# Kernel tuning notes

Measured on AMD Instinct MI355X. Metric: run time of the kernel, lower is better.

## Reference

```python
import math
import jax, jax.numpy as jnp
import numpy as np

WH, WW = 7, 7
NUM_HEADS = 16


def _relative_position_index(wh, ww):
    # Static int index table, identical to the torch buffer construction.
    ch, cw = np.arange(wh), np.arange(ww)
    coords = np.stack(np.meshgrid(ch, cw, indexing='ij'))        # (2, wh, ww)
    cf = coords.reshape(2, -1)                                    # (2, N)
    rel = cf[:, :, None] - cf[:, None, :]                         # (2, N, N)
    rel = rel.transpose(1, 2, 0).copy()                           # (N, N, 2)
    rel[:, :, 0] += wh - 1
    rel[:, :, 1] += ww - 1
    rel[:, :, 0] *= 2 * ww - 1
    return rel.sum(-1)                                            # (N, N) int


def setup_inputs() -> dict:
    key = jax.random.key(0)
    ks = jax.random.split(key, 7)
    B_, N, C = 2048, WH * WW, 512
    nW = 64
    s = 1.0 / math.sqrt(C)
    return {
        'x': jax.random.normal(ks[0], (B_, N, C), jnp.float32),
        'mask': jax.random.normal(ks[1], (nW, N, N), jnp.float32),
        'qkv_w': jax.random.normal(ks[2], (3 * C, C), jnp.float32) * s,
        'qkv_b': jax.random.normal(ks[3], (3 * C,), jnp.float32) * 0.02,
        'proj_w': jax.random.normal(ks[4], (C, C), jnp.float32) * s,
        'proj_b': jax.random.normal(ks[5], (C,), jnp.float32) * 0.02,
        'bias_table': jax.random.normal(ks[6], (2 * WH - 1, 2 * WW - 1, NUM_HEADS), jnp.float32) * 0.02,
    }


def reference(x, mask, qkv_w, qkv_b, proj_w, proj_b, bias_table):
    B_, N, C = x.shape
    nH = NUM_HEADS
    hd = C // nH
    scale = math.sqrt(hd)  # self.scale = qk_scale or sqrt(head_dim)

    qkv = x @ qkv_w.T + qkv_b                                   # (B_, N, 3C)
    qkv = qkv.reshape(B_, N, 3, nH, hd).transpose(2, 0, 3, 1, 4)  # (3, B_, nH, N, hd)
    q, k, v = qkv[0], qkv[1], qkv[2]

    attn = jnp.einsum('bhnd,bhmd->bhnm', q, k) / scale           # (B_, nH, N, N)

    idx = _relative_position_index(WH, WW).reshape(-1)            # (N*N,) static
    bias = bias_table.reshape(-1, nH)[idx].reshape(N, N, nH)      # gather
    attn = attn + bias.transpose(2, 0, 1)[None]                   # (B_, nH, N, N)

    nW = mask.shape[0]
    attn = attn.reshape(B_ // nW, nW, nH, N, N) + mask[None, :, None]
    attn = attn.reshape(B_, nH, N, N)

    attn = jax.nn.softmax(attn, axis=-1)
    out = jnp.einsum('bhnm,bhmd->bhnd', attn, v)                  # (B_, nH, N, hd)
    out = out.transpose(0, 2, 1, 3).reshape(B_, N, C)
    return out @ proj_w.T + proj_b
```

## Files before the change

### kernel.cpp

```cpp
#include <hip/hip_runtime.h>
#include <hip/hip_bf16.h>


typedef __bf16  bf16x8 __attribute__((ext_vector_type(8)));
typedef float   f32x4  __attribute__((ext_vector_type(4)));

#define B_TOT   2048
#define NTOK    49
#define CDIM    512
#define NHEAD   16
#define HDIM    32
#define MROWS   (B_TOT * NTOK)
#define QKVN    (3 * CDIM)

__device__ __forceinline__ void load_lds16(const void* gptr, void* lptr) {
    __builtin_amdgcn_global_load_lds(
        (const __attribute__((address_space(1))) unsigned int*)gptr,
        (__attribute__((address_space(3))) unsigned int*)lptr,
        16, 0, 0);
}
__device__ __forceinline__ void load_lds4(const void* gptr, void* lptr) {
    __builtin_amdgcn_global_load_lds(
        (const __attribute__((address_space(1))) unsigned int*)gptr,
        (__attribute__((address_space(3))) unsigned int*)lptr,
        4, 0, 0);
}

__global__ void cvt_f32_bf16(const float* __restrict__ in,
                             __hip_bfloat16* __restrict__ out, int n4) {
    int idx = blockIdx.x * blockDim.x + threadIdx.x;
    int stride = gridDim.x * blockDim.x;
    for (int i = idx; i < n4; i += stride) {
        float4 f = ((const float4*)in)[i];
        union { __hip_bfloat16 h[4]; ushort4 u; } c;
        c.h[0] = __float2bfloat16(f.x);
        c.h[1] = __float2bfloat16(f.y);
        c.h[2] = __float2bfloat16(f.z);
        c.h[3] = __float2bfloat16(f.w);
        ((ushort4*)out)[i] = c.u;
    }
}

#define BARR    asm volatile("s_barrier" ::: "memory")
#define WAITV(N) asm volatile("s_waitcnt vmcnt(" #N ")" ::: "memory")
#define MFMA16(av, bv, cv) __builtin_amdgcn_mfma_f32_16x16x32_bf16(av, bv, cv, 0, 0, 0)

template <typename OutT>
__global__ __launch_bounds__(512, 2) void gemm256(
    const __hip_bfloat16* __restrict__ A,
    const __hip_bfloat16* __restrict__ B,
    const float* __restrict__ bias,
    OutT* __restrict__ C,
    int M, int N, int K, int nbx, int cpx)
{
    extern __shared__ __align__(16) char smem[];
    char* sA = smem;
    char* sB = smem + 65536;

    const int NT = K >> 6;

    const int tid  = threadIdx.x;
    const int lane = tid & 63;
    const int wave = tid >> 6;
    const int wm   = wave >> 2;
    const int wn   = wave & 3;
    const int l16  = lane & 15;
    const int quad = lane >> 4;

    const int id = blockIdx.x;
    const int sw = (id & 7) * cpx + (id >> 3);
    const int mb = sw / nbx;
    const int nb = sw - mb * nbx;
    const int m0 = mb << 8;
    const int n0 = nb << 8;

    const int srow = tid >> 3;
    const int scg  = ((tid & 7) << 3) ^ ((srow & 7) << 3);
    const __hip_bfloat16* Asrc = A + (size_t)(m0 + srow) * K + scg;
    const __hip_bfloat16* Bsrc = B + (size_t)(n0 + srow) * K + scg;
    char* dAl = sA + tid * 16;
    char* dBl = sB + tid * 16;

#define STG_A(t2, h) \
    { load_lds16(Asrc + (size_t)(h) * 128 * K + (t2) * 64,            \
                 dAl + ((t2) & 1) * 32768 + (h) * 16384);             \
      load_lds16(Asrc + ((size_t)(h) * 128 + 64) * K + (t2) * 64,     \
                 dAl + ((t2) & 1) * 32768 + (h) * 16384 + 8192); }
#define STG_B(t2, h) \
    { load_lds16(Bsrc + (size_t)(h) * 128 * K + (t2) * 64,            \
                 dBl + ((t2) & 1) * 32768 + (h) * 16384);             \
      load_lds16(Bsrc + ((size_t)(h) * 128 + 64) * K + (t2) * 64,     \
                 dBl + ((t2) & 1) * 32768 + (h) * 16384 + 8192); }

    STG_A(0, 0); STG_A(0, 1); STG_B(0, 0); STG_B(0, 1);
    STG_A(1, 0); STG_A(1, 1); STG_B(1, 0); STG_B(1, 1);
    WAITV(8);
    BARR;

    const int c0 = (quad * 16) ^ ((l16 & 7) << 4);
    const int c1 = c0 ^ 64;

    f32x4 acc[8][4] = {};

#define CLUSTER(mfa, mfb)                                                  \
    {                                                                      \
        bf16x8 xk0 = *(const bf16x8*)(pA + (mfa) * 2048 + c0);             \
        bf16x8 xk1 = *(const bf16x8*)(pA + (mfa) * 2048 + c1);             \
        bf16x8 yk0 = *(const bf16x8*)(pA + (mfb) * 2048 + c0);             \
        bf16x8 yk1 = *(const bf16x8*)(pA + (mfb) * 2048 + c1);             \
        __builtin_amdgcn_s_setprio(1);                                     \
        _Pragma("unroll")                                                  \
        for (int nf = 0; nf < 4; ++nf) {                                   \
            acc[mfa][nf] = MFMA16(xk0, Bf0[nf], acc[mfa][nf]);             \
            acc[mfa][nf] = MFMA16(xk1, Bf1[nf], acc[mfa][nf]);             \
            acc[mfb][nf] = MFMA16(yk0, Bf0[nf], acc[mfb][nf]);             \
            acc[mfb][nf] = MFMA16(yk1, Bf1[nf], acc[mfb][nf]);             \
        }                                                                  \
        __builtin_amdgcn_s_setprio(0);                                     \
    }

#pragma unroll 2
    for (int t = 0; t < NT; ++t) {
        const int sl = (t & 1) * 32768;
        const char* pA = sA + sl + wm * 16384 + l16 * 128;
        const char* pB = sB + sl + (wn >> 1) * 16384 + ((wn & 1) * 64 + l16) * 128;

        bf16x8 Bf0[4], Bf1[4];
#pragma unroll
        for (int nf = 0; nf < 4; ++nf) {
            Bf0[nf] = *(const bf16x8*)(pB + nf * 2048 + c0);
            Bf1[nf] = *(const bf16x8*)(pB + nf * 2048 + c1);
        }

        CLUSTER(0, 1);
        CLUSTER(2, 3);
        CLUSTER(4, 5);

        bf16x8 a6k0 = *(const bf16x8*)(pA + 6 * 2048 + c0);
        bf16x8 a6k1 = *(const bf16x8*)(pA + 6 * 2048 + c1);
        bf16x8 a7k0 = *(const bf16x8*)(pA + 7 * 2048 + c0);
        bf16x8 a7k1 = *(const bf16x8*)(pA + 7 * 2048 + c1);
        asm volatile("s_waitcnt lgkmcnt(0)" ::: "memory");
        BARR;

        if (t + 2 < NT) { STG_A(t + 2, 0); STG_A(t + 2, 1);
                          STG_B(t + 2, 0); STG_B(t + 2, 1); }

        __builtin_amdgcn_s_setprio(1);
#pragma unroll
        for (int nf = 0; nf < 4; ++nf) {
            acc[6][nf] = MFMA16(a6k0, Bf0[nf], acc[6][nf]);
            acc[6][nf] = MFMA16(a6k1, Bf1[nf], acc[6][nf]);
            acc[7][nf] = MFMA16(a7k0, Bf0[nf], acc[7][nf]);
            acc[7][nf] = MFMA16(a7k1, Bf1[nf], acc[7][nf]);
        }
        __builtin_amdgcn_s_setprio(0);

        if (t + 2 < NT) { WAITV(8); }
        else if (t + 1 < NT) { WAITV(0); }
        BARR;
    }
#undef CLUSTER
#undef STG_A
#undef STG_B

#pragma unroll
    for (int i = 0; i < 8; ++i) {
#pragma unroll
        for (int jj = 0; jj < 4; ++jj) {
            const int col = n0 + wn * 64 + jj * 16 + l16;
            const float bv = bias[col];
#pragma unroll
            for (int rr = 0; rr < 4; ++rr) {
                const int row = m0 + wm * 128 + i * 16 + quad * 4 + rr;
                const float val = acc[i][jj][rr] + bv;
                if constexpr (sizeof(OutT) == 2)
                    C[(size_t)row * N + col] = __float2bfloat16(val);
                else
                    C[(size_t)row * N + col] = val;
            }
        }
    }
}

#define QS_OFF   0
#define KS_OFF   12544
#define VS_OFF   25088
#define BIAS_OFF 41472
#define MASK_OFF 42824
#define SMEM_BYTES 52432

__global__ __launch_bounds__(256) void attn_mfma(
    const __hip_bfloat16* __restrict__ qkv,
    const float* __restrict__ mask,
    const float* __restrict__ bias_table,
    __hip_bfloat16* __restrict__ out)
{
    __shared__ __align__(16) char smem[SMEM_BYTES];

    const int tid  = threadIdx.x;
    const int lane = tid & 63;
    const int w    = tid >> 6;
    const int l16  = lane & 15;
    const int quad = lane >> 4;
    const int b    = blockIdx.x >> 2;
    const int hq   = blockIdx.x & 3;

    {
        const long rowbase = (long)b * NTOK * QKVN;
        for (int e = tid; e < 2352; e += 256) {
            const int m   = e / 784;
            const int rr  = e - m * 784;
            const int tok = rr >> 4, seg = rr & 15;
            const int segl = seg ^ (tok & 7);
            const __hip_bfloat16* src =
                qkv + rowbase + (long)tok * QKVN + m * 512 + hq * 128 + segl * 8;
            load_lds16(src, smem + e * 16);
        }
        for (int e = tid; e < 960; e += 256)
            ((unsigned int*)(smem + VS_OFF + 49 * 256))[e] = 0u;
        const float* msrc = mask + (long)(b & 63) * (NTOK * NTOK);
        for (int e = tid; e < NTOK * NTOK; e += 256)
            load_lds4(msrc + e, smem + MASK_OFF + e * 4);
        __hip_bfloat16* sb = (__hip_bfloat16*)(smem + BIAS_OFF);
        for (int e = tid; e < 676; e += 256) {
            const int w2 = e / 169, rel = e - w2 * 169;
            sb[e] = __float2bfloat16(bias_table[rel * NHEAD + hq * 4 + w2]);
        }
    }
    __syncthreads();

    const int fro = (w * 64 + quad * 16) ^ ((l16 & 7) << 4);
    bf16x8 af[4], bf[4];
#pragma unroll
    for (int t = 0; t < 4; ++t) {
        const int tok = t * 16 + l16;
        af[t] = *(const bf16x8*)(smem + KS_OFF + tok * 256 + fro);
        bf[t] = *(const bf16x8*)(smem + QS_OFF + tok * 256 + fro);
    }
    f32x4 acc[4][4] = {};
#pragma unroll
    for (int i = 0; i < 4; ++i)
#pragma unroll
        for (int j = 0; j < 4; ++j)
            acc[i][j] = __builtin_amdgcn_mfma_f32_16x16x32_bf16(
                af[i], bf[j], acc[i][j], 0, 0, 0);
    __syncthreads();

    const float scale = 0.17677669529663687f;
    const float* smf = (const float*)(smem + MASK_OFF);
    const __hip_bfloat16* sb = (const __hip_bfloat16*)(smem + BIAS_OFF);
    const int quad4 = quad * 4;

    int kp[4][4];
#pragma unroll
    for (int i = 0; i < 4; ++i)
#pragma unroll
        for (int r = 0; r < 4; ++r) {
            const int k  = i * 16 + quad4 + r;
            const int rj = k / 7, cj = k - rj * 7;
            kp[i][r] = (6 - rj) * 13 + (6 - cj);
        }

    char* pbase = smem + w * 6272;
#pragma unroll
    for (int j = 0; j < 4; ++j) {
        const int q   = j * 16 + l16;
        const bool qok = q < NTOK;
        const int ri  = q / 7, ci = q - ri * 7;
        const int qp  = ri * 13 + ci;
        const int mrow = q * NTOK;
        float mx = -1e30f;
#pragma unroll
        for (int i = 0; i < 4; ++i)
#pragma unroll
            for (int r = 0; r < 4; ++r) {
                const int k = i * 16 + quad4 + r;
                float v;
                if (qok && k < NTOK) {
                    v = fmaf(acc[i][j][r], scale,
                             __bfloat162float(sb[w * 169 + qp + kp[i][r]]) + smf[mrow + k]);
                } else {
                    v = -1e30f;
                }
                acc[i][j][r] = v;
                mx = fmaxf(mx, v);
            }
        mx = fmaxf(mx, __shfl_xor(mx, 16));
        mx = fmaxf(mx, __shfl_xor(mx, 32));
        float s = 0.f;
#pragma unroll
        for (int i = 0; i < 4; ++i)
#pragma unroll
            for (int r = 0; r < 4; ++r) {
                const float ev = __expf(acc[i][j][r] - mx);
                acc[i][j][r] = ev;
                s += ev;
            }
        s += __shfl_xor(s, 16);
        s += __shfl_xor(s, 32);
        const float inv = 1.0f / s;
        if (qok) {
            char* prow = pbase + q * 128;
            const int xr = (q & 7) << 4;
#pragma unroll
            for (int i = 0; i < 4; ++i) {
                union { __hip_bfloat16 h[4]; uint2 u; } pk;
#pragma unroll
                for (int r = 0; r < 4; ++r)
                    pk.h[r] = __float2bfloat16(acc[i][j][r] * inv);
                *(uint2*)(prow + ((i * 32 + quad * 8) ^ xr)) = pk.u;
            }
        }
    }
    __syncthreads();

    bf16x8 pa[4][2];
#pragma unroll
    for (int mt = 0; mt < 4; ++mt) {
        const int q  = mt * 16 + l16;
        const int xr = (q & 7) << 4;
#pragma unroll
        for (int ks = 0; ks < 2; ++ks)
            pa[mt][ks] = *(const bf16x8*)(pbase + q * 128 + ((ks * 64 + quad * 16) ^ xr));
    }
    bf16x8 vb[2][2];
#pragma unroll
    for (int dt = 0; dt < 2; ++dt)
#pragma unroll
        for (int ks = 0; ks < 2; ++ks)
#pragma unroll
            for (int e = 0; e < 8; ++e) {
                const int key = ks * 32 + quad * 8 + e;
                const int dby = (w * 32 + dt * 16 + l16) * 2;
                vb[dt][ks][e] = *(const __bf16*)(smem + VS_OFF + key * 256 + (dby ^ (e << 4)));
            }
    f32x4 o[4][2] = {};
#pragma unroll
    for (int mt = 0; mt < 4; ++mt)
#pragma unroll
        for (int dt = 0; dt < 2; ++dt)
#pragma unroll
            for (int ks = 0; ks < 2; ++ks)
                o[mt][dt] = __builtin_amdgcn_mfma_f32_16x16x32_bf16(
                    pa[mt][ks], vb[dt][ks], o[mt][dt], 0, 0, 0);

    const long obase = (long)b * NTOK * CDIM + hq * 128 + w * 32;
#pragma unroll
    for (int mt = 0; mt < 4; ++mt)
#pragma unroll
        for (int r = 0; r < 4; ++r) {
            const int q = mt * 16 + quad4 + r;
            if (q < NTOK) {
                const long rb = obase + (long)q * CDIM;
#pragma unroll
                for (int dt = 0; dt < 2; ++dt)
                    out[rb + dt * 16 + l16] = __float2bfloat16(o[mt][dt][r]);
            }
        }
}

extern "C" void kernel_launch(void* const* d_in, const int* in_sizes, int n_in,
                              void* d_out, int out_size, void* d_ws, size_t ws_size,
                              hipStream_t stream) {
    const float* x          = (const float*)d_in[0];
    const float* mask       = (const float*)d_in[1];
    const float* qkv_w      = (const float*)d_in[2];
    const float* qkv_b      = (const float*)d_in[3];
    const float* proj_w     = (const float*)d_in[4];
    const float* proj_b     = (const float*)d_in[5];
    const float* bias_table = (const float*)d_in[6];

    char* ws = (char*)d_ws;
    __hip_bfloat16* xb   = (__hip_bfloat16*)(ws);
    __hip_bfloat16* qw   = (__hip_bfloat16*)(ws + 102760448);
    __hip_bfloat16* pw   = (__hip_bfloat16*)(ws + 104333312);
    __hip_bfloat16* qkvb = (__hip_bfloat16*)(ws + 104857600);
    __hip_bfloat16* ao   = xb;

    static int attr_done = 0;
    if (!attr_done) {
        hipFuncSetAttribute(
            reinterpret_cast<const void*>(&gemm256<__hip_bfloat16>),
            hipFuncAttributeMaxDynamicSharedMemorySize, 131072);
        hipFuncSetAttribute(
            reinterpret_cast<const void*>(&gemm256<float>),
            hipFuncAttributeMaxDynamicSharedMemorySize, 131072);
        attr_done = 1;
    }

    cvt_f32_bf16<<<32768, 256, 0, stream>>>(x, xb, (MROWS * CDIM) / 4);
    cvt_f32_bf16<<<768,   256, 0, stream>>>(qkv_w, qw, (QKVN * CDIM) / 4);
    cvt_f32_bf16<<<256,   256, 0, stream>>>(proj_w, pw, (CDIM * CDIM) / 4);

    gemm256<__hip_bfloat16><<<2352, 512, 131072, stream>>>(
        xb, qw, qkv_b, qkvb, MROWS, QKVN, CDIM, 6, 294);

    attn_mfma<<<B_TOT * 4, 256, 0, stream>>>(qkvb, mask, bias_table, ao);

    gemm256<float><<<784, 512, 131072, stream>>>(
        ao, pw, proj_b, (float*)d_out, MROWS, CDIM, CDIM, 2, 98);
}
```

Baseline: 754.2 us.

## Restructure GEMM main loop into quadrant phases with interleaved staged loads

Replaces the double-buffered K loop with a fully unrolled 8-step loop, where each step is split into four quadrant phases (M-half by N-half). Each phase issues its LDS reads, launches part of the next tile's global-to-LDS copies, then runs its MFMAs between barriers. The intent is to spread global loads and LDS traffic across the compute so they overlap more evenly with the MFMAs. The loop now hardcodes K=512 (8 tiles of 64) and adds many more barriers, which could cost sync overhead, and it drops the generic NT so other K values are no longer handled.

New measurement: 713.8 us. -5.4%, faster.

```diff
diff --git a/kernel.cpp b/kernel.cpp
--- a/kernel.cpp
+++ b/kernel.cpp
@@ -43,6 +43,7 @@
 
 #define BARR    asm volatile("s_barrier" ::: "memory")
 #define WAITV(N) asm volatile("s_waitcnt vmcnt(" #N ")" ::: "memory")
+#define LGKM0   asm volatile("s_waitcnt lgkmcnt(0)" ::: "memory")
 #define MFMA16(av, bv, cv) __builtin_amdgcn_mfma_f32_16x16x32_bf16(av, bv, cv, 0, 0, 0)
 
 template <typename OutT>
@@ -57,8 +58,6 @@
     char* sA = smem;
     char* sB = smem + 65536;
 
-    const int NT = K >> 6;
-
     const int tid  = threadIdx.x;
     const int lane = tid & 63;
     const int wave = tid >> 6;
@@ -93,74 +92,77 @@
                  dBl + ((t2) & 1) * 32768 + (h) * 16384 + 8192); }
 
     STG_A(0, 0); STG_A(0, 1); STG_B(0, 0); STG_B(0, 1);
-    STG_A(1, 0); STG_A(1, 1); STG_B(1, 0); STG_B(1, 1);
-    WAITV(8);
+    STG_B(1, 0); STG_B(1, 1);
+    WAITV(4);
     BARR;
 
+    const char* pA0 = sA + wm * 16384 + l16 * 128;
+    const char* pA1 = pA0 + 32768;
+    const char* pB0 = sB + (wn >> 1) * 16384 + (wn & 1) * 8192 + l16 * 128;
+    const char* pB1 = pB0 + 32768;
     const int c0 = (quad * 16) ^ ((l16 & 7) << 4);
     const int c1 = c0 ^ 64;
 
+    bf16x8 ar[8], b0r[4], b1r[4];
     f32x4 acc[8][4] = {};
 
-#define CLUSTER(mfa, mfb)                                                  \
-    {                                                                      \
-        bf16x8 xk0 = *(const bf16x8*)(pA + (mfa) * 2048 + c0);             \
-        bf16x8 xk1 = *(const bf16x8*)(pA + (mfa) * 2048 + c1);             \
-        bf16x8 yk0 = *(const bf16x8*)(pA + (mfb) * 2048 + c0);             \
-        bf16x8 yk1 = *(const bf16x8*)(pA + (mfb) * 2048 + c1);             \
-        __builtin_amdgcn_s_setprio(1);                                     \
-        _Pragma("unroll")                                                  \
-        for (int nf = 0; nf < 4; ++nf) {                                   \
-            acc[mfa][nf] = MFMA16(xk0, Bf0[nf], acc[mfa][nf]);             \
-            acc[mfa][nf] = MFMA16(xk1, Bf1[nf], acc[mfa][nf]);             \
-            acc[mfb][nf] = MFMA16(yk0, Bf0[nf], acc[mfb][nf]);             \
-            acc[mfb][nf] = MFMA16(yk1, Bf1[nf], acc[mfb][nf]);             \
-        }                                                                  \
-        __builtin_amdgcn_s_setprio(0);                                     \
-    }
-
-#pragma unroll 2
-    for (int t = 0; t < NT; ++t) {
-        const int sl = (t & 1) * 32768;
-        const char* pA = sA + sl + wm * 16384 + l16 * 128;
-        const char* pB = sB + sl + (wn >> 1) * 16384 + ((wn & 1) * 64 + l16) * 128;
-
-        bf16x8 Bf0[4], Bf1[4];
-#pragma unroll
-        for (int nf = 0; nf < 4; ++nf) {
-            Bf0[nf] = *(const bf16x8*)(pB + nf * 2048 + c0);
-            Bf1[nf] = *(const bf16x8*)(pB + nf * 2048 + c1);
-        }
-
-        CLUSTER(0, 1);
-        CLUSTER(2, 3);
-        CLUSTER(4, 5);
-
-        bf16x8 a6k0 = *(const bf16x8*)(pA + 6 * 2048 + c0);
-        bf16x8 a6k1 = *(const bf16x8*)(pA + 6 * 2048 + c1);
-        bf16x8 a7k0 = *(const bf16x8*)(pA + 7 * 2048 + c0);
-        bf16x8 a7k1 = *(const bf16x8*)(pA + 7 * 2048 + c1);
-        asm volatile("s_waitcnt lgkmcnt(0)" ::: "memory");
+#define PH_READS_A(pA, mh)                                                  \
+    _Pragma("unroll") for (int i = 0; i < 4; ++i) {                         \
+        ar[2 * i]     = *(const bf16x8*)((pA) + (mh) * 8192 + i * 2048 + c0); \
+        ar[2 * i + 1] = *(const bf16x8*)((pA) + (mh) * 8192 + i * 2048 + c1); \
+    }
+#define PH_READS_B(pB, nh, br)                                              \
+    _Pragma("unroll") for (int j = 0; j < 2; ++j) {                         \
+        br[2 * j]     = *(const bf16x8*)((pB) + (nh) * 4096 + j * 2048 + c0); \
+        br[2 * j + 1] = *(const bf16x8*)((pB) + (nh) * 4096 + j * 2048 + c1); \
+    }
+#define PH_MFMA(mh, nh, br)                                                 \
+    __builtin_amdgcn_s_setprio(1);                                          \
+    _Pragma("unroll") for (int i = 0; i < 4; ++i)                           \
+    _Pragma("unroll") for (int j = 0; j < 2; ++j) {                         \
+        acc[(mh) * 4 + i][(nh) * 2 + j] = MFMA16(                           \
+            ar[2 * i], br[2 * j], acc[(mh) * 4 + i][(nh) * 2 + j]);         \
+        acc[(mh) * 4 + i][(nh) * 2 + j] = MFMA16(                           \
+            ar[2 * i + 1], br[2 * j + 1], acc[(mh) * 4 + i][(nh) * 2 + j]); \
+    }                                                                       \
+    __builtin_amdgcn_s_setprio(0);
+
+#pragma unroll
+    for (int it = 0; it < 4; ++it) {
+        const int t = 2 * it, u = t + 1;
+        const bool more = (it < 3);
+
+        PH_READS_A(pA0, 0); PH_READS_B(pB0, 0, b0r);
+        STG_A(u, 0);
+        BARR; LGKM0; PH_MFMA(0, 0, b0r); BARR;
+        PH_READS_B(pB0, 1, b1r);
+        STG_A(u, 1);
+        BARR; LGKM0; PH_MFMA(0, 1, b1r); BARR;
+        PH_READS_A(pA0, 1);
+        if (more) STG_B(t + 2, 0);
+        BARR; LGKM0; PH_MFMA(1, 0, b0r); BARR;
+        if (more) STG_B(t + 2, 1);
+        BARR; PH_MFMA(1, 1, b1r);
+        if (more) { WAITV(4); } else { WAITV(0); }
         BARR;
 
-        if (t + 2 < NT) { STG_A(t + 2, 0); STG_A(t + 2, 1);
-                          STG_B(t + 2, 0); STG_B(t + 2, 1); }
-
-        __builtin_amdgcn_s_setprio(1);
-#pragma unroll
-        for (int nf = 0; nf < 4; ++nf) {
-            acc[6][nf] = MFMA16(a6k0, Bf0[nf], acc[6][nf]);
-            acc[6][nf] = MFMA16(a6k1, Bf1[nf], acc[6][nf]);
-            acc[7][nf] = MFMA16(a7k0, Bf0[nf], acc[7][nf]);
-            acc[7][nf] = MFMA16(a7k1, Bf1[nf], acc[7][nf]);
-        }
-        __builtin_amdgcn_s_setprio(0);
-
-        if (t + 2 < NT) { WAITV(8); }
-        else if (t + 1 < NT) { WAITV(0); }
+        PH_READS_A(pA1, 0); PH_READS_B(pB1, 0, b0r);
+        if (more) STG_A(t + 2, 0);
+        BARR; LGKM0; PH_MFMA(0, 0, b0r); BARR;
+        PH_READS_B(pB1, 1, b1r);
+        if (more) STG_A(t + 2, 1);
+        BARR; LGKM0; PH_MFMA(0, 1, b1r); BARR;
+        PH_READS_A(pA1, 1);
+        if (more) STG_B(t + 3, 0);
+        BARR; LGKM0; PH_MFMA(1, 0, b0r); BARR;
+        if (more) STG_B(t + 3, 1);
+        BARR; PH_MFMA(1, 1, b1r);
+        if (more) { WAITV(4); }
         BARR;
     }
-#undef CLUSTER
+#undef PH_READS_A
+#undef PH_READS_B
+#undef PH_MFMA
 #undef STG_A
 #undef STG_B
 
```
